# Optimization experiments

Hardware: AMD Instinct MI355X
Metric: run time of the kernel (lower is better)

## Reference

```python
import jax, jax.numpy as jnp
import numpy as np

TEMP = 2.0   # NTXent uses a hardcoded temperature of 2, not the ctor's 0.07
EPS = 1e-8   # F.cosine_similarity eps


def setup_inputs() -> dict:
    key = jax.random.key(0)
    k1, _ = jax.random.split(key)
    x = jax.random.normal(k1, (8192, 256), dtype=jnp.float32)
    unused = jnp.zeros((1,), dtype=jnp.int32)
    return {"x": x, "unused": unused}


def _cos_matrix(a, b):
    # pairwise cosine similarity: [N, N]
    na = jnp.linalg.norm(a, axis=-1)
    nb = jnp.linalg.norm(b, axis=-1)
    dots = a @ b.T
    return dots / jnp.maximum(na[:, None] * nb[None, :], EPS)


def reference(x, unused):
    n = x.shape[0] // 2
    p, q = x[:n], x[n:]  # anchor, positive

    s_pp = _cos_matrix(p, p)
    s_pn = _cos_matrix(p, q)
    s_nn = _cos_matrix(q, q)
    s_np = _cos_matrix(q, p)

    # double loop i, j in [i, n): upper triangle including diagonal
    mask = jnp.triu(jnp.ones((n, n), dtype=bool))

    exp_sum = (jnp.exp(s_pp / TEMP) + jnp.exp(s_pn / TEMP)
               + jnp.exp(s_nn / TEMP) + jnp.exp(s_np / TEMP))
    sim_all = jnp.sum(jnp.where(mask, exp_sum, 0.0))

    sim_s = jnp.sum(jnp.exp(jnp.diagonal(s_pn) / TEMP))

    return -jnp.log(sim_s / sim_all)
```

## Files before the change

kernel.cpp:

```cpp
#include <hip/hip_runtime.h>

#define DIM    256
#define NROWS  8192
#define NHALF  4096
#define NTILE  64
#define NBLK   ((NTILE * (NTILE + 1)) / 2)
#define RSTRIDE 128

using i32x4  = __attribute__((ext_vector_type(4))) int;
using i32x8  = __attribute__((ext_vector_type(8))) int;
using f32x16 = __attribute__((ext_vector_type(16))) float;

struct i32x8_pair { i32x4 lo, hi; };

__device__ __forceinline__ unsigned fp4q(float v) {
  float a = fabsf(v);
  unsigned s = (__builtin_bit_cast(unsigned, v) >> 31) << 3;
  unsigned c = a < 0.25f ? 0u : a < 0.75f ? 1u : a < 1.25f ? 2u : a < 1.75f ? 3u
             : a < 2.50f ? 4u : a < 3.50f ? 5u : a < 5.00f ? 6u : 7u;
  return s | c;
}

__global__ __launch_bounds__(256) void normalize_k(const float* __restrict__ x,
                                                   unsigned char* __restrict__ z4) {
  const int row  = blockIdx.x * 4 + (threadIdx.x >> 6);
  const int lane = threadIdx.x & 63;
  float4 v = ((const float4*)(x + (size_t)row * DIM))[lane];
  float ss = v.x * v.x + v.y * v.y + v.z * v.z + v.w * v.w;
#pragma unroll
  for (int off = 32; off > 0; off >>= 1) ss += __shfl_xor(ss, off, 64);
  float rn = rsqrtf(fmaxf(ss, 1e-24f)) * 16.0f;
  unsigned c0 = fp4q(v.x * rn), c1 = fp4q(v.y * rn);
  unsigned c2 = fp4q(v.z * rn), c3 = fp4q(v.w * rn);
  unsigned short pk = (unsigned short)((c0 | (c1 << 4)) | ((c2 | (c3 << 4)) << 8));
  ((unsigned short*)(z4 + (size_t)row * RSTRIDE))[lane] = pk;
}

__global__ __launch_bounds__(256, 4) void gram_k(const unsigned char* __restrict__ z4,
                                                 double2* __restrict__ partial) {
  __shared__ unsigned char As[128 * RSTRIDE];
  __shared__ unsigned char Bs[128 * RSTRIDE];
  __shared__ float red[8];

  const int bid = blockIdx.x;
  int bi = (int)((129.0 - sqrt(129.0 * 129.0 - 8.0 * (double)bid)) * 0.5);
  while ((bi * (129 - bi)) / 2 > bid) --bi;
  while (((bi + 1) * (128 - bi)) / 2 <= bid) ++bi;
  const int bj = bi + (bid - (bi * (129 - bi)) / 2);

  const int tid   = threadIdx.x;
  const int lane  = tid & 63;
  const int w     = tid >> 6;
  const int wr    = w >> 1, wc = w & 1;
  const int l31   = lane & 31;
  const int khalf = lane >> 5;

  const size_t rowA0 = (size_t)bi * 128;
  const size_t rowB0 = (size_t)bj * 128;

#pragma unroll
  for (int i = 0; i < 4; ++i) {
    int c   = i * 256 + tid;
    int row = c >> 3;
    int cb  = c & 7;
    int gcb = cb ^ (row & 7);
    const unsigned char* ga = z4 + (rowA0 + row) * RSTRIDE + gcb * 16;
    const unsigned char* gb = z4 + (rowB0 + row) * RSTRIDE + gcb * 16;
    __builtin_amdgcn_global_load_lds(
        (const __attribute__((address_space(1))) void*)ga,
        (__attribute__((address_space(3))) void*)&As[(size_t)(i * 256 + (tid & ~63)) * 16],
        16, 0, 0);
    __builtin_amdgcn_global_load_lds(
        (const __attribute__((address_space(1))) void*)gb,
        (__attribute__((address_space(3))) void*)&Bs[(size_t)(i * 256 + (tid & ~63)) * 16],
        16, 0, 0);
  }
  __syncthreads();

  f32x16 acc_f[2][2] = {};
  const i32x4 zero4 = {0, 0, 0, 0};
#pragma unroll
  for (int kc = 0; kc < 4; ++kc) {
    const int ch = kc * 2 + khalf;
    i32x8 a[2], b[2];
#pragma unroll
    for (int t = 0; t < 2; ++t) {
      int mr = wr * 64 + t * 32 + l31;
      i32x8_pair pa = { *(const i32x4*)&As[mr * RSTRIDE + (ch ^ (mr & 7)) * 16], zero4 };
      a[t] = __builtin_bit_cast(i32x8, pa);
      int nr = wc * 64 + t * 32 + l31;
      i32x8_pair pb = { *(const i32x4*)&Bs[nr * RSTRIDE + (ch ^ (nr & 7)) * 16], zero4 };
      b[t] = __builtin_bit_cast(i32x8, pb);
    }
#pragma unroll
    for (int ti = 0; ti < 2; ++ti)
#pragma unroll
      for (int tj = 0; tj < 2; ++tj)
        acc_f[ti][tj] = __builtin_amdgcn_mfma_scale_f32_32x32x64_f8f6f4(
            a[ti], b[tj], acc_f[ti][tj],
            4, 4,
            0, 0x7B7B7B7B,
            0, 0x7B7B7B7B);
  }

  const bool tdiag = (bi == bj);
  const bool sdiag = (bj == bi + 32);
  float lsum = 0.0f, dsum = 0.0f;
  if (tdiag || sdiag) {
#pragma unroll
    for (int ti = 0; ti < 2; ++ti)
#pragma unroll
      for (int tj = 0; tj < 2; ++tj)
#pragma unroll
        for (int r = 0; r < 16; ++r) {
          float e = __expf(acc_f[ti][tj][r] * 0.5f);
          lsum += e;
          int row_l = (r & 3) + 8 * (r >> 2) + 4 * khalf;
          if (wr == wc && ti == tj && row_l == l31) dsum += e;
        }
  } else {
#pragma unroll
    for (int ti = 0; ti < 2; ++ti)
#pragma unroll
      for (int tj = 0; tj < 2; ++tj)
#pragma unroll
        for (int r = 0; r < 16; ++r)
          lsum += __expf(acc_f[ti][tj][r] * 0.5f);
  }
#pragma unroll
  for (int off = 32; off > 0; off >>= 1) lsum += __shfl_xor(lsum, off, 64);
  if (tdiag || sdiag) {
#pragma unroll
    for (int off = 32; off > 0; off >>= 1) dsum += __shfl_xor(dsum, off, 64);
  }
  if (lane == 0) { red[w] = lsum; red[4 + w] = dsum; }
  __syncthreads();

  if (tid == 0) {
    float l  = red[0] + red[1] + red[2] + red[3];
    float dd = red[4] + red[5] + red[6] + red[7];
    double2 v;
    v.x = tdiag ? (double)l + (double)dd : 2.0 * (double)l;
    v.y = sdiag ? (double)dd : 0.0;
    partial[bid] = v;
  }
}

__global__ __launch_bounds__(256) void reduce_k(const double2* __restrict__ partial,
                                               float* __restrict__ out) {
  __shared__ double redS[4], redD[4];
  double s = 0.0, ss = 0.0;
  for (int i = threadIdx.x; i < NBLK; i += 256) {
    double2 v = partial[i];
    s += v.x; ss += v.y;
  }
#pragma unroll
  for (int off = 32; off > 0; off >>= 1) {
    s  += __shfl_xor(s,  off, 64);
    ss += __shfl_xor(ss, off, 64);
  }
  const int w = threadIdx.x >> 6;
  if ((threadIdx.x & 63) == 0) { redS[w] = s; redD[w] = ss; }
  __syncthreads();
  if (threadIdx.x == 0) {
    double S  = redS[0] + redS[1] + redS[2] + redS[3];
    double sd = redD[0] + redD[1] + redD[2] + redD[3];
    out[0] = (float)(log(0.5 * S + sd) - log(sd));
  }
}

extern "C" void kernel_launch(void* const* d_in, const int* in_sizes, int n_in,
                              void* d_out, int out_size, void* d_ws, size_t ws_size,
                              hipStream_t stream) {
  const float* x    = (const float*)d_in[0];
  unsigned char* z4 = (unsigned char*)d_ws;
  double2* partial  = (double2*)((char*)d_ws + (size_t)NROWS * RSTRIDE);
  float* out        = (float*)d_out;

  normalize_k<<<dim3(NROWS / 4), dim3(256), 0, stream>>>(x, z4);
  gram_k<<<dim3(NBLK), dim3(256), 0, stream>>>(z4, partial);
  reduce_k<<<dim3(1), dim3(256), 0, stream>>>(partial, out);
}
```

Baseline: 75.19 us.

## Make gram kernel persistent with double-buffered LDS tile prefetch

Replaces one-block-per-tile launch of 2080 blocks with 512 persistent blocks that each process 4-5 triangular tiles, double-buffering the A/B tiles in LDS so the next tile's global-to-LDS loads overlap the current tile's MFMA and exp work. Sums accumulate in per-wave doubles and are written as per-wave partials, which removes the per-tile LDS reduction and block sync. Doubling LDS lowers occupancy to 2 blocks per CU, and the final tiles create some load imbalance across blocks.

```diff
diff --git a/kernel.cpp b/kernel.cpp
--- a/kernel.cpp
+++ b/kernel.cpp
@@ -2,9 +2,10 @@
 
 #define DIM    256
 #define NROWS  8192
-#define NHALF  4096
 #define NTILE  64
 #define NBLK   ((NTILE * (NTILE + 1)) / 2)
+#define NB     512
+#define NPART  (NB * 4)
 #define RSTRIDE 128
 
 using i32x4  = __attribute__((ext_vector_type(4))) int;
@@ -21,6 +22,14 @@
   return s | c;
 }
 
+__device__ __forceinline__ void tile_rc(int t, int& bi, int& bj) {
+  int i = (int)((129.0 - sqrt(129.0 * 129.0 - 8.0 * (double)t)) * 0.5);
+  while ((i * (129 - i)) / 2 > t) --i;
+  while (((i + 1) * (128 - i)) / 2 <= t) ++i;
+  bi = i;
+  bj = i + (t - (i * (129 - i)) / 2);
+}
+
 __global__ __launch_bounds__(256) void normalize_k(const float* __restrict__ x,
                                                    unsigned char* __restrict__ z4) {
   const int row  = blockIdx.x * 4 + (threadIdx.x >> 6);
@@ -36,17 +45,10 @@
   ((unsigned short*)(z4 + (size_t)row * RSTRIDE))[lane] = pk;
 }
 
-__global__ __launch_bounds__(256, 4) void gram_k(const unsigned char* __restrict__ z4,
+__global__ __launch_bounds__(256, 2) void gram_k(const unsigned char* __restrict__ z4,
                                                  double2* __restrict__ partial) {
-  __shared__ unsigned char As[128 * RSTRIDE];
-  __shared__ unsigned char Bs[128 * RSTRIDE];
-  __shared__ float red[8];
-
-  const int bid = blockIdx.x;
-  int bi = (int)((129.0 - sqrt(129.0 * 129.0 - 8.0 * (double)bid)) * 0.5);
-  while ((bi * (129 - bi)) / 2 > bid) --bi;
-  while (((bi + 1) * (128 - bi)) / 2 <= bid) ++bi;
-  const int bj = bi + (bid - (bi * (129 - bi)) / 2);
+  __shared__ unsigned char As[2][128 * RSTRIDE];
+  __shared__ unsigned char Bs[2][128 * RSTRIDE];
 
   const int tid   = threadIdx.x;
   const int lane  = tid & 63;
@@ -55,94 +57,118 @@
   const int l31   = lane & 31;
   const int khalf = lane >> 5;
 
-  const size_t rowA0 = (size_t)bi * 128;
-  const size_t rowB0 = (size_t)bj * 128;
-
-#pragma unroll
-  for (int i = 0; i < 4; ++i) {
-    int c   = i * 256 + tid;
-    int row = c >> 3;
-    int cb  = c & 7;
-    int gcb = cb ^ (row & 7);
-    const unsigned char* ga = z4 + (rowA0 + row) * RSTRIDE + gcb * 16;
-    const unsigned char* gb = z4 + (rowB0 + row) * RSTRIDE + gcb * 16;
-    __builtin_amdgcn_global_load_lds(
-        (const __attribute__((address_space(1))) void*)ga,
-        (__attribute__((address_space(3))) void*)&As[(size_t)(i * 256 + (tid & ~63)) * 16],
-        16, 0, 0);
-    __builtin_amdgcn_global_load_lds(
-        (const __attribute__((address_space(1))) void*)gb,
-        (__attribute__((address_space(3))) void*)&Bs[(size_t)(i * 256 + (tid & ~63)) * 16],
-        16, 0, 0);
-  }
-  __syncthreads();
-
-  f32x16 acc_f[2][2] = {};
+  const int b  = blockIdx.x;
+  const int nt = 4 + (b < (NBLK - 4 * NB) ? 1 : 0);
+
+  auto stage = [&](int s, int t) {
+    int sbi, sbj; tile_rc(t, sbi, sbj);
+    const size_t rA = (size_t)sbi * 128, rB = (size_t)sbj * 128;
+#pragma unroll
+    for (int i = 0; i < 4; ++i) {
+      int c   = i * 256 + tid;
+      int row = c >> 3;
+      int cb  = c & 7;
+      int gcb = cb ^ (row & 7);
+      const unsigned char* ga = z4 + (rA + row) * RSTRIDE + gcb * 16;
+      const unsigned char* gb = z4 + (rB + row) * RSTRIDE + gcb * 16;
+      __builtin_amdgcn_global_load_lds(
+          (const __attribute__((address_space(1))) void*)ga,
+          (__attribute__((address_space(3))) void*)&As[s][(size_t)(i * 256 + (tid & ~63)) * 16],
+          16, 0, 0);
+      __builtin_amdgcn_global_load_lds(
+          (const __attribute__((address_space(1))) void*)gb,
+          (__attribute__((address_space(3))) void*)&Bs[s][(size_t)(i * 256 + (tid & ~63)) * 16],
+          16, 0, 0);
+    }
+  };
+
+  stage(0, b);
+  stage(1, b + NB);
+  asm volatile("s_waitcnt vmcnt(8)" ::: "memory");
+  __builtin_amdgcn_s_barrier();
+  __builtin_amdgcn_sched_barrier(0);
+
+  double accS = 0.0, accD = 0.0;
   const i32x4 zero4 = {0, 0, 0, 0};
-#pragma unroll
-  for (int kc = 0; kc < 4; ++kc) {
-    const int ch = kc * 2 + khalf;
-    i32x8 a[2], b[2];
-#pragma unroll
-    for (int t = 0; t < 2; ++t) {
-      int mr = wr * 64 + t * 32 + l31;
-      i32x8_pair pa = { *(const i32x4*)&As[mr * RSTRIDE + (ch ^ (mr & 7)) * 16], zero4 };
-      a[t] = __builtin_bit_cast(i32x8, pa);
-      int nr = wc * 64 + t * 32 + l31;
-      i32x8_pair pb = { *(const i32x4*)&Bs[nr * RSTRIDE + (ch ^ (nr & 7)) * 16], zero4 };
-      b[t] = __builtin_bit_cast(i32x8, pb);
-    }
-#pragma unroll
-    for (int ti = 0; ti < 2; ++ti)
-#pragma unroll
-      for (int tj = 0; tj < 2; ++tj)
-        acc_f[ti][tj] = __builtin_amdgcn_mfma_scale_f32_32x32x64_f8f6f4(
-            a[ti], b[tj], acc_f[ti][tj],
-            4, 4,
-            0, 0x7B7B7B7B,
-            0, 0x7B7B7B7B);
-  }
-
-  const bool tdiag = (bi == bj);
-  const bool sdiag = (bj == bi + 32);
-  float lsum = 0.0f, dsum = 0.0f;
-  if (tdiag || sdiag) {
-#pragma unroll
-    for (int ti = 0; ti < 2; ++ti)
-#pragma unroll
-      for (int tj = 0; tj < 2; ++tj)
-#pragma unroll
-        for (int r = 0; r < 16; ++r) {
-          float e = __expf(acc_f[ti][tj][r] * 0.5f);
-          lsum += e;
-          int row_l = (r & 3) + 8 * (r >> 2) + 4 * khalf;
-          if (wr == wc && ti == tj && row_l == l31) dsum += e;
-        }
-  } else {
-#pragma unroll
-    for (int ti = 0; ti < 2; ++ti)
-#pragma unroll
-      for (int tj = 0; tj < 2; ++tj)
-#pragma unroll
-        for (int r = 0; r < 16; ++r)
-          lsum += __expf(acc_f[ti][tj][r] * 0.5f);
-  }
-#pragma unroll
-  for (int off = 32; off > 0; off >>= 1) lsum += __shfl_xor(lsum, off, 64);
-  if (tdiag || sdiag) {
-#pragma unroll
-    for (int off = 32; off > 0; off >>= 1) dsum += __shfl_xor(dsum, off, 64);
-  }
-  if (lane == 0) { red[w] = lsum; red[4 + w] = dsum; }
-  __syncthreads();
-
-  if (tid == 0) {
-    float l  = red[0] + red[1] + red[2] + red[3];
-    float dd = red[4] + red[5] + red[6] + red[7];
-    double2 v;
-    v.x = tdiag ? (double)l + (double)dd : 2.0 * (double)l;
-    v.y = sdiag ? (double)dd : 0.0;
-    partial[bid] = v;
+
+  for (int k = 0; ; ++k) {
+    const int cur = k & 1;
+    int bik, bjk; tile_rc(b + k * NB, bik, bjk);
+
+    f32x16 acc_f[2][2] = {};
+#pragma unroll
+    for (int kc = 0; kc < 4; ++kc) {
+      const int ch = kc * 2 + khalf;
+      i32x8 a[2], bf[2];
+#pragma unroll
+      for (int t = 0; t < 2; ++t) {
+        int mr = wr * 64 + t * 32 + l31;
+        i32x8_pair pa = { *(const i32x4*)&As[cur][mr * RSTRIDE + (ch ^ (mr & 7)) * 16], zero4 };
+        a[t] = __builtin_bit_cast(i32x8, pa);
+        int nr = wc * 64 + t * 32 + l31;
+        i32x8_pair pb = { *(const i32x4*)&Bs[cur][nr * RSTRIDE + (ch ^ (nr & 7)) * 16], zero4 };
+        bf[t] = __builtin_bit_cast(i32x8, pb);
+      }
+#pragma unroll
+      for (int ti = 0; ti < 2; ++ti)
+#pragma unroll
+        for (int tj = 0; tj < 2; ++tj)
+          acc_f[ti][tj] = __builtin_amdgcn_mfma_scale_f32_32x32x64_f8f6f4(
+              a[ti], bf[tj], acc_f[ti][tj],
+              4, 4,
+              0, 0x7B7B7B7B,
+              0, 0x7B7B7B7B);
+    }
+
+    const bool tdiag = (bik == bjk);
+    const bool sdiag = (bjk == bik + 32);
+    float lsum = 0.0f, dsum = 0.0f;
+    if (tdiag || sdiag) {
+#pragma unroll
+      for (int ti = 0; ti < 2; ++ti)
+#pragma unroll
+        for (int tj = 0; tj < 2; ++tj)
+#pragma unroll
+          for (int r = 0; r < 16; ++r) {
+            float e = __expf(acc_f[ti][tj][r] * 0.5f);
+            lsum += e;
+            int row_l = (r & 3) + 8 * (r >> 2) + 4 * khalf;
+            if (wr == wc && ti == tj && row_l == l31) dsum += e;
+          }
+    } else {
+#pragma unroll
+      for (int ti = 0; ti < 2; ++ti)
+#pragma unroll
+        for (int tj = 0; tj < 2; ++tj)
+#pragma unroll
+          for (int r = 0; r < 16; ++r)
+            lsum += __expf(acc_f[ti][tj][r] * 0.5f);
+    }
+    accS += tdiag ? (double)lsum + (double)dsum : 2.0 * (double)lsum;
+    if (sdiag) accD += (double)dsum;
+
+    if (k == nt - 1) break;
+
+    __builtin_amdgcn_s_barrier();
+    __builtin_amdgcn_sched_barrier(0);
+    if (k + 2 < nt) {
+      stage(cur, b + (k + 2) * NB);
+      asm volatile("s_waitcnt vmcnt(8)" ::: "memory");
+    } else {
+      asm volatile("s_waitcnt vmcnt(0)" ::: "memory");
+    }
+    __builtin_amdgcn_s_barrier();
+    __builtin_amdgcn_sched_barrier(0);
+  }
+
+#pragma unroll
+  for (int off = 32; off > 0; off >>= 1) {
+    accS += __shfl_xor(accS, off, 64);
+    accD += __shfl_xor(accD, off, 64);
+  }
+  if (lane == 0) {
+    double2 v; v.x = accS; v.y = accD;
+    partial[b * 4 + w] = v;
   }
 }
 
@@ -150,7 +176,7 @@
                                                float* __restrict__ out) {
   __shared__ double redS[4], redD[4];
   double s = 0.0, ss = 0.0;
-  for (int i = threadIdx.x; i < NBLK; i += 256) {
+  for (int i = threadIdx.x; i < NPART; i += 256) {
     double2 v = partial[i];
     s += v.x; ss += v.y;
   }
@@ -178,6 +204,6 @@
   float* out        = (float*)d_out;
 
   normalize_k<<<dim3(NROWS / 4), dim3(256), 0, stream>>>(x, z4);
-  gram_k<<<dim3(NBLK), dim3(256), 0, stream>>>(z4, partial);
+  gram_k<<<dim3(NB), dim3(256), 0, stream>>>(z4, partial);
   reduce_k<<<dim3(1), dim3(256), 0, stream>>>(partial, out);
 }
```

New measurement: 77.51 us. 1.03x slower.

## Store FP4 rows in chunk-planar layout and load MFMA operands directly from global

Applied to the files above, without the earlier changes.

The normalize kernel now writes the quantized FP4 data as eight 16-byte chunk planes, so each lane's MFMA operand is one contiguous 16-byte global load. The gram kernel drops the LDS staging, the swizzle and the barrier, and reads A/B fragments straight from global memory (L2). It also lowers the occupancy hint in launch bounds from 4 to 3 and replaces __expf with a raw v_exp_f32 using a pre-folded scale. This removes LDS traffic and synchronisation but relies on cache hits for reused tiles, and its wave-level loads may coalesce less well.

```diff
diff --git a/kernel.cpp b/kernel.cpp
--- a/kernel.cpp
+++ b/kernel.cpp
@@ -1,11 +1,10 @@
 #include <hip/hip_runtime.h>
 
-#define DIM    256
-#define NROWS  8192
-#define NHALF  4096
-#define NTILE  64
-#define NBLK   ((NTILE * (NTILE + 1)) / 2)
-#define RSTRIDE 128
+#define DIM     256
+#define NROWS   8192
+#define NTILE   64
+#define NBLK    ((NTILE * (NTILE + 1)) / 2)
+#define CHPLANE ((size_t)NROWS * 16)
 
 using i32x4  = __attribute__((ext_vector_type(4))) int;
 using i32x8  = __attribute__((ext_vector_type(8))) int;
@@ -21,6 +20,21 @@
   return s | c;
 }
 
+__device__ __forceinline__ void tile_rc(int t, int& bi, int& bj) {
+  int i = (int)((129.0 - sqrt(129.0 * 129.0 - 8.0 * (double)t)) * 0.5);
+  while ((i * (129 - i)) / 2 > t) --i;
+  while (((i + 1) * (128 - i)) / 2 <= t) ++i;
+  bi = i;
+  bj = i + (t - (i * (129 - i)) / 2);
+}
+
+__device__ __forceinline__ float exp_half(float x) {
+  float t = x * 0.7213475204444817f;
+  float r;
+  asm("v_exp_f32 %0, %1" : "=v"(r) : "v"(t));
+  return r;
+}
+
 __global__ __launch_bounds__(256) void normalize_k(const float* __restrict__ x,
                                                    unsigned char* __restrict__ z4) {
   const int row  = blockIdx.x * 4 + (threadIdx.x >> 6);
@@ -33,20 +47,13 @@
   unsigned c0 = fp4q(v.x * rn), c1 = fp4q(v.y * rn);
   unsigned c2 = fp4q(v.z * rn), c3 = fp4q(v.w * rn);
   unsigned short pk = (unsigned short)((c0 | (c1 << 4)) | ((c2 | (c3 << 4)) << 8));
-  ((unsigned short*)(z4 + (size_t)row * RSTRIDE))[lane] = pk;
+  *(unsigned short*)(z4 + (size_t)(lane >> 3) * CHPLANE
+                        + (size_t)row * 16 + ((2 * lane) & 14)) = pk;
 }
 
-__global__ __launch_bounds__(256, 4) void gram_k(const unsigned char* __restrict__ z4,
+__global__ __launch_bounds__(256, 3) void gram_k(const unsigned char* __restrict__ z4,
                                                  double2* __restrict__ partial) {
-  __shared__ unsigned char As[128 * RSTRIDE];
-  __shared__ unsigned char Bs[128 * RSTRIDE];
   __shared__ float red[8];
-
-  const int bid = blockIdx.x;
-  int bi = (int)((129.0 - sqrt(129.0 * 129.0 - 8.0 * (double)bid)) * 0.5);
-  while ((bi * (129 - bi)) / 2 > bid) --bi;
-  while (((bi + 1) * (128 - bi)) / 2 <= bid) ++bi;
-  const int bj = bi + (bid - (bi * (129 - bi)) / 2);
 
   const int tid   = threadIdx.x;
   const int lane  = tid & 63;
@@ -55,41 +62,25 @@
   const int l31   = lane & 31;
   const int khalf = lane >> 5;
 
-  const size_t rowA0 = (size_t)bi * 128;
-  const size_t rowB0 = (size_t)bj * 128;
+  int bi, bj; tile_rc(blockIdx.x, bi, bj);
 
-#pragma unroll
-  for (int i = 0; i < 4; ++i) {
-    int c   = i * 256 + tid;
-    int row = c >> 3;
-    int cb  = c & 7;
-    int gcb = cb ^ (row & 7);
-    const unsigned char* ga = z4 + (rowA0 + row) * RSTRIDE + gcb * 16;
-    const unsigned char* gb = z4 + (rowB0 + row) * RSTRIDE + gcb * 16;
-    __builtin_amdgcn_global_load_lds(
-        (const __attribute__((address_space(1))) void*)ga,
-        (__attribute__((address_space(3))) void*)&As[(size_t)(i * 256 + (tid & ~63)) * 16],
-        16, 0, 0);
-    __builtin_amdgcn_global_load_lds(
-        (const __attribute__((address_space(1))) void*)gb,
-        (__attribute__((address_space(3))) void*)&Bs[(size_t)(i * 256 + (tid & ~63)) * 16],
-        16, 0, 0);
-  }
-  __syncthreads();
+  const unsigned char* baseA = z4 + (size_t)khalf * CHPLANE
+                             + ((size_t)bi * 128 + wr * 64 + l31) * 16;
+  const unsigned char* baseB = z4 + (size_t)khalf * CHPLANE
+                             + ((size_t)bj * 128 + wc * 64 + l31) * 16;
 
   f32x16 acc_f[2][2] = {};
   const i32x4 zero4 = {0, 0, 0, 0};
 #pragma unroll
   for (int kc = 0; kc < 4; ++kc) {
-    const int ch = kc * 2 + khalf;
     i32x8 a[2], b[2];
 #pragma unroll
     for (int t = 0; t < 2; ++t) {
-      int mr = wr * 64 + t * 32 + l31;
-      i32x8_pair pa = { *(const i32x4*)&As[mr * RSTRIDE + (ch ^ (mr & 7)) * 16], zero4 };
+      i32x8_pair pa = { *(const i32x4*)(baseA + (size_t)(2 * kc) * CHPLANE + t * 32 * 16),
+                        zero4 };
       a[t] = __builtin_bit_cast(i32x8, pa);
-      int nr = wc * 64 + t * 32 + l31;
-      i32x8_pair pb = { *(const i32x4*)&Bs[nr * RSTRIDE + (ch ^ (nr & 7)) * 16], zero4 };
+      i32x8_pair pb = { *(const i32x4*)(baseB + (size_t)(2 * kc) * CHPLANE + t * 32 * 16),
+                        zero4 };
       b[t] = __builtin_bit_cast(i32x8, pb);
     }
 #pragma unroll
@@ -113,7 +104,7 @@
       for (int tj = 0; tj < 2; ++tj)
 #pragma unroll
         for (int r = 0; r < 16; ++r) {
-          float e = __expf(acc_f[ti][tj][r] * 0.5f);
+          float e = exp_half(acc_f[ti][tj][r]);
           lsum += e;
           int row_l = (r & 3) + 8 * (r >> 2) + 4 * khalf;
           if (wr == wc && ti == tj && row_l == l31) dsum += e;
@@ -125,7 +116,7 @@
       for (int tj = 0; tj < 2; ++tj)
 #pragma unroll
         for (int r = 0; r < 16; ++r)
-          lsum += __expf(acc_f[ti][tj][r] * 0.5f);
+          lsum += exp_half(acc_f[ti][tj][r]);
   }
 #pragma unroll
   for (int off = 32; off > 0; off >>= 1) lsum += __shfl_xor(lsum, off, 64);
@@ -142,7 +133,7 @@
     double2 v;
     v.x = tdiag ? (double)l + (double)dd : 2.0 * (double)l;
     v.y = sdiag ? (double)dd : 0.0;
-    partial[bid] = v;
+    partial[blockIdx.x] = v;
   }
 }
 
@@ -174,7 +165,7 @@
                               hipStream_t stream) {
   const float* x    = (const float*)d_in[0];
   unsigned char* z4 = (unsigned char*)d_ws;
-  double2* partial  = (double2*)((char*)d_ws + (size_t)NROWS * RSTRIDE);
+  double2* partial  = (double2*)((char*)d_ws + 8 * CHPLANE);
   float* out        = (float*)d_out;
 
   normalize_k<<<dim3(NROWS / 4), dim3(256), 0, stream>>>(x, z4);
```

New measurement: 74.33 us, median of 2. No clear change (-1.1%).
